# Kernel tuning notes

Measured on AMD Instinct MI355X. Metric: run time of the kernel, lower is better.

Reference implementation:

```python
import math
import jax, jax.numpy as jnp
import numpy as np

B, L, S, H, E, D = 4, 2048, 2048, 8, 64, 64

def setup_inputs() -> dict:
    key = jax.random.key(0)
    kq, kk, kv = jax.random.split(key, 3)
    return {
        "queries": jax.random.normal(kq, (B, L, H, E), dtype=jnp.float32),
        "keys": jax.random.normal(kk, (B, S, H, E), dtype=jnp.float32),
        "values": jax.random.normal(kv, (B, S, H, D), dtype=jnp.float32),
    }

def reference(queries, keys, values):
    E_ = queries.shape[-1]
    scale = 1.0 / math.sqrt(E_)
    # scores: [B, H, L, S]
    scores = jnp.einsum('blhe,bshe->bhls', queries, keys)
    A = jax.nn.softmax(scale * scores, axis=-1)
    # dropout omitted (eval mode / p=0.0)
    out = jnp.einsum('bhls,bshd->blhd', A, values)
    return out
```

## Files before the change

kernel.cpp:

```cpp
#include <hip/hip_runtime.h>
#include <hip/hip_bf16.h>


#define BNUM 4
#define LLEN 2048
#define SLEN 2048
#define HNUM 8
#define EDIM 64

typedef __attribute__((ext_vector_type(8))) short s16x8;
typedef __attribute__((ext_vector_type(8))) _Float16 hf16x8;
typedef __attribute__((ext_vector_type(2))) __fp16 fp16x2;
typedef __attribute__((ext_vector_type(4))) float f32x4;

__device__ __forceinline__ short f2h(float f) {
    union { _Float16 h; short s; } u;
    u.h = (_Float16)f;
    return u.s;
}

__device__ __forceinline__ s16x8 pk8(float4 a, float4 b) {
    union { fp16x2 h[4]; s16x8 v; } u;
    u.h[0] = __builtin_amdgcn_cvt_pkrtz(a.x, a.y);
    u.h[1] = __builtin_amdgcn_cvt_pkrtz(a.z, a.w);
    u.h[2] = __builtin_amdgcn_cvt_pkrtz(b.x, b.y);
    u.h[3] = __builtin_amdgcn_cvt_pkrtz(b.z, b.w);
    return u.v;
}

#if __has_builtin(__builtin_amdgcn_global_load_lds)
#define HAVE_GLL 1
#else
#define HAVE_GLL 0
#endif

__device__ __forceinline__ void stage16(const short* g, short* l) {
#if HAVE_GLL
    __builtin_amdgcn_global_load_lds(
        (const __attribute__((address_space(1))) void*)g,
        (__attribute__((address_space(3))) void*)l, 16, 0, 0);
#else
    *(s16x8*)l = *(const s16x8*)g;
#endif
}

__global__ __launch_bounds__(256)
void prep(const float* __restrict__ Kg, const float* __restrict__ Vg,
          short* __restrict__ Kc, short* __restrict__ Vt)
{
    __shared__ short tile[EDIM][80];
    if (blockIdx.y == 0) {
        const int t = blockIdx.x * 256 + threadIdx.x;
        const int e8 = t & 7;
        const int tmp = t >> 3;
        const int h = tmp & 7;
        const int tmp2 = tmp >> 3;
        const int s = tmp2 & (SLEN - 1);
        const int b = tmp2 >> 11;
        const float4* src = (const float4*)(Kg + (((size_t)(b * SLEN + s) * HNUM + h) * EDIM + e8 * 8));
        float4 a = src[0], bb = src[1];
        *(s16x8*)(Kc + ((size_t)((b * HNUM + h) * SLEN + s) * EDIM + e8 * 8)) = pk8(a, bb);
    } else {
        if (blockIdx.x >= 1024) return;
        const int x = blockIdx.x;
        const int s0 = (x & 31) * 64;
        const int bh = x >> 5;
        const int b = bh >> 3, h = bh & 7;
        {
            const int sr = threadIdx.x >> 2, dc = (threadIdx.x & 3) * 16;
            const float4* src = (const float4*)(Vg + (((size_t)(b * SLEN + s0 + sr) * HNUM + h) * EDIM + dc));
            #pragma unroll
            for (int j4 = 0; j4 < 4; ++j4) {
                float4 a = src[j4];
                tile[dc + j4*4 + 0][sr] = f2h(a.x);
                tile[dc + j4*4 + 1][sr] = f2h(a.y);
                tile[dc + j4*4 + 2][sr] = f2h(a.z);
                tile[dc + j4*4 + 3][sr] = f2h(a.w);
            }
        }
        __syncthreads();
        {
            const int dr = threadIdx.x >> 2, sc = (threadIdx.x & 3) * 16;
            short* dst = Vt + ((size_t)((b * HNUM + h) * EDIM + dr) * SLEN + s0 + sc);
            *(s16x8*)dst       = *(const s16x8*)&tile[dr][sc];
            *(s16x8*)(dst + 8) = *(const s16x8*)&tile[dr][sc + 8];
        }
    }
}

__global__ __launch_bounds__(512, 4)
void fa_fwd(const float* __restrict__ Qg, const short* __restrict__ Kc,
            const short* __restrict__ Vt, float* __restrict__ Og)
{
    __shared__ float sOf[128 * 68];
    __shared__ float sL[2][128];
    short* sKV = (short*)sOf;

    const int tid  = threadIdx.x;
    const int wave = tid >> 6;
    const int sw   = wave & 1;
    const int qh   = wave >> 1;
    const int lane = tid & 63;
    const int m    = lane & 15;
    const int quad = lane >> 4;

    const int lin  = (int)blockIdx.x;
    const int logi = ((lin & 7) << 6) + (lin >> 3);
    const int qx = logi & 15;
    const int h  = (logi >> 4) & 7;
    const int b  = logi >> 7;
    const int qbase = qx * 128;
    const int bh = b * HNUM + h;

    const short* Kbh = Kc + (size_t)bh * SLEN * EDIM;
    const short* Vbh = Vt + (size_t)bh * EDIM * SLEN;

    const int l3 = lane >> 3;
    const int ksrcE = (wave * 32 + l3) * EDIM + ((lane & 7) ^ (l3 & 3)) * 8;
    const int ksrcO = (wave * 32 + l3) * EDIM + ((lane & 7) ^ (4 + (l3 & 3))) * 8;
    const int vsrcB = (lane >> 2) * SLEN + wave * 32 + ((lane & 3) ^ ((lane >> 2) & 3)) * 8;
    short* kdstB = sKV + (wave * 256 + lane) * 8;
    short* vdstB = sKV + 4096 + (wave * 256 + lane) * 8;

#define STAGE_TILE(s0)                                                        \
    do {                                                                      \
        _Pragma("unroll")                                                     \
        for (int p = 0; p < 4; ++p) {                                         \
            const int ks = ((p & 1) ? ksrcO : ksrcE) + (p >> 1) * 1024 + (p & 1) * 512; \
            stage16(Kbh + (size_t)(s0) * EDIM + ks, kdstB + p * 512);         \
            stage16(Vbh + (s0) + vsrcB + p * 16 * SLEN, vdstB + p * 512);     \
        }                                                                     \
    } while (0)

    const float csc = 0.18033688011112042f;
    hf16x8 qfrag[2][2];
    #pragma unroll
    for (int qtl = 0; qtl < 2; ++qtl)
        #pragma unroll
        for (int kb = 0; kb < 2; ++kb) {
            const int qtg = qh * 2 + qtl;
            const float* qp = Qg + ((size_t)(b * LLEN + qbase + qtg * 16 + m) * HNUM + h) * EDIM
                              + kb * 32 + quad * 8;
            float4 x0 = *(const float4*)qp;
            float4 x1 = *(const float4*)(qp + 4);
            float4 y0 = {x0.x*csc, x0.y*csc, x0.z*csc, x0.w*csc};
            float4 y1 = {x1.x*csc, x1.y*csc, x1.z*csc, x1.w*csc};
            union { s16x8 s; hf16x8 hh; } u;
            u.s = pk8(y0, y1);
            qfrag[qtl][kb] = u.hh;
        }

    const int gk  = ((m >> 2) & 1) * 4 + (m & 3);
    const int pi0 = 8 * (m >> 2) + (m & 3);
    const int kOff00 = (sw * 32 + pi0)     * 64 + ((quad)     ^ gk) * 8;
    const int kOff01 = (sw * 32 + pi0)     * 64 + ((4 + quad) ^ gk) * 8;
    const int kOff10 = (sw * 32 + pi0 + 4) * 64 + ((quad)     ^ gk) * 8;
    const int kOff11 = (sw * 32 + pi0 + 4) * 64 + ((4 + quad) ^ gk) * 8;
    const int vOffB  = 4096 + sw * 2048 + m * 32 + ((quad ^ (m & 3)) * 8);

    hf16x8 vones;
    #pragma unroll
    for (int j = 0; j < 8; ++j) vones[j] = (_Float16)1.0f;

    f32x4 oacc[2][4];
    f32x4 lacc[2];
    #pragma unroll
    for (int i = 0; i < 2; ++i) {
        #pragma unroll
        for (int j = 0; j < 4; ++j) oacc[i][j] = (f32x4){0.f, 0.f, 0.f, 0.f};
        lacc[i] = (f32x4){0.f, 0.f, 0.f, 0.f};
    }

    if (wave < 2) STAGE_TILE(0);
    __syncthreads();

    for (int s0 = 0; s0 < SLEN; s0 += 64) {
        hf16x8 kf00 = *(const hf16x8*)(sKV + kOff00);
        hf16x8 kf01 = *(const hf16x8*)(sKV + kOff01);
        hf16x8 kf10 = *(const hf16x8*)(sKV + kOff10);
        hf16x8 kf11 = *(const hf16x8*)(sKV + kOff11);
        hf16x8 vf0 = *(const hf16x8*)(sKV + vOffB);
        hf16x8 vf1 = *(const hf16x8*)(sKV + vOffB + 512);
        hf16x8 vf2 = *(const hf16x8*)(sKV + vOffB + 1024);
        hf16x8 vf3 = *(const hf16x8*)(sKV + vOffB + 1536);

        __syncthreads();

        if (s0 + 64 < SLEN && wave < 2) STAGE_TILE(s0 + 64);

        #pragma unroll
        for (int qtl = 0; qtl < 2; ++qtl) {
            f32x4 a0 = {0.f, 0.f, 0.f, 0.f};
            f32x4 a1 = {0.f, 0.f, 0.f, 0.f};
            a0 = __builtin_amdgcn_mfma_f32_16x16x32_f16(kf00, qfrag[qtl][0], a0, 0, 0, 0);
            a0 = __builtin_amdgcn_mfma_f32_16x16x32_f16(kf01, qfrag[qtl][1], a0, 0, 0, 0);
            a1 = __builtin_amdgcn_mfma_f32_16x16x32_f16(kf10, qfrag[qtl][0], a1, 0, 0, 0);
            a1 = __builtin_amdgcn_mfma_f32_16x16x32_f16(kf11, qfrag[qtl][1], a1, 0, 0, 0);
            float p0 = __builtin_amdgcn_exp2f(a0[0]);
            float p1 = __builtin_amdgcn_exp2f(a0[1]);
            float p2 = __builtin_amdgcn_exp2f(a0[2]);
            float p3 = __builtin_amdgcn_exp2f(a0[3]);
            float p4 = __builtin_amdgcn_exp2f(a1[0]);
            float p5 = __builtin_amdgcn_exp2f(a1[1]);
            float p6 = __builtin_amdgcn_exp2f(a1[2]);
            float p7 = __builtin_amdgcn_exp2f(a1[3]);
            union { fp16x2 h2[4]; hf16x8 v; } pu;
            pu.h2[0] = __builtin_amdgcn_cvt_pkrtz(p0, p1);
            pu.h2[1] = __builtin_amdgcn_cvt_pkrtz(p2, p3);
            pu.h2[2] = __builtin_amdgcn_cvt_pkrtz(p4, p5);
            pu.h2[3] = __builtin_amdgcn_cvt_pkrtz(p6, p7);
            hf16x8 pf = pu.v;
            lacc[qtl] = __builtin_amdgcn_mfma_f32_16x16x32_f16(pf, vones, lacc[qtl], 0, 0, 0);
            oacc[qtl][0] = __builtin_amdgcn_mfma_f32_16x16x32_f16(pf, vf0, oacc[qtl][0], 0, 0, 0);
            oacc[qtl][1] = __builtin_amdgcn_mfma_f32_16x16x32_f16(pf, vf1, oacc[qtl][1], 0, 0, 0);
            oacc[qtl][2] = __builtin_amdgcn_mfma_f32_16x16x32_f16(pf, vf2, oacc[qtl][2], 0, 0, 0);
            oacc[qtl][3] = __builtin_amdgcn_mfma_f32_16x16x32_f16(pf, vf3, oacc[qtl][3], 0, 0, 0);
        }

        __syncthreads();
    }

    if (m == 0) {
        #pragma unroll
        for (int qtl = 0; qtl < 2; ++qtl)
            #pragma unroll
            for (int r = 0; r < 4; ++r)
                sL[sw][(qh * 2 + qtl) * 16 + quad * 4 + r] = lacc[qtl][r];
    }
    __syncthreads();

    if (sw == 0) {
        #pragma unroll
        for (int qtl = 0; qtl < 2; ++qtl)
            #pragma unroll
            for (int dt = 0; dt < 4; ++dt)
                #pragma unroll
                for (int r = 0; r < 4; ++r)
                    sOf[((qh * 2 + qtl) * 16 + quad * 4 + r) * 68 + dt * 16 + m] = oacc[qtl][dt][r];
    }
    __syncthreads();
    if (sw == 1) {
        #pragma unroll
        for (int qtl = 0; qtl < 2; ++qtl)
            #pragma unroll
            for (int dt = 0; dt < 4; ++dt)
                #pragma unroll
                for (int r = 0; r < 4; ++r)
                    sOf[((qh * 2 + qtl) * 16 + quad * 4 + r) * 68 + dt * 16 + m] += oacc[qtl][dt][r];
    }
    __syncthreads();

    {
        const int q = tid >> 2;
        const int dcol = (tid & 3) * 16;
        const float l = sL[0][q] + sL[1][q];
        const float inv = 1.0f / l;
        float* orow = Og + ((size_t)(b * LLEN + qbase + q) * HNUM + h) * EDIM + dcol;
        #pragma unroll
        for (int j = 0; j < 4; ++j) {
            float4 v = *(const float4*)(sOf + q * 68 + dcol + j * 4);
            v.x *= inv; v.y *= inv; v.z *= inv; v.w *= inv;
            *(float4*)(orow + j * 4) = v;
        }
    }
}

extern "C" void kernel_launch(void* const* d_in, const int* in_sizes, int n_in,
                              void* d_out, int out_size, void* d_ws, size_t ws_size,
                              hipStream_t stream) {
    const float* Q = (const float*)d_in[0];
    const float* K = (const float*)d_in[1];
    const float* V = (const float*)d_in[2];
    float* O = (float*)d_out;

    const size_t NE = (size_t)BNUM * LLEN * HNUM * EDIM;
    short* Kc = (short*)d_ws;
    short* Vt = Kc + NE;

    prep<<<dim3(2048, 2), dim3(256), 0, stream>>>(K, V, Kc, Vt);
    fa_fwd<<<dim3(512), dim3(512), 0, stream>>>(Q, Kc, Vt, O);
}
```

Before: 137.4 us.

## Fuse K/V fp16 conversion and V transpose into attention kernel, drop prep pass

```diff
diff --git a/kernel.cpp b/kernel.cpp
--- a/kernel.cpp
+++ b/kernel.cpp
@@ -7,6 +7,7 @@
 #define SLEN 2048
 #define HNUM 8
 #define EDIM 64
+#define RSTRIDE (HNUM * EDIM)
 
 typedef __attribute__((ext_vector_type(8))) short s16x8;
 typedef __attribute__((ext_vector_type(8))) _Float16 hf16x8;
@@ -28,69 +29,9 @@
     return u.v;
 }
 
-#if __has_builtin(__builtin_amdgcn_global_load_lds)
-#define HAVE_GLL 1
-#else
-#define HAVE_GLL 0
-#endif
-
-__device__ __forceinline__ void stage16(const short* g, short* l) {
-#if HAVE_GLL
-    __builtin_amdgcn_global_load_lds(
-        (const __attribute__((address_space(1))) void*)g,
-        (__attribute__((address_space(3))) void*)l, 16, 0, 0);
-#else
-    *(s16x8*)l = *(const s16x8*)g;
-#endif
-}
-
-__global__ __launch_bounds__(256)
-void prep(const float* __restrict__ Kg, const float* __restrict__ Vg,
-          short* __restrict__ Kc, short* __restrict__ Vt)
-{
-    __shared__ short tile[EDIM][80];
-    if (blockIdx.y == 0) {
-        const int t = blockIdx.x * 256 + threadIdx.x;
-        const int e8 = t & 7;
-        const int tmp = t >> 3;
-        const int h = tmp & 7;
-        const int tmp2 = tmp >> 3;
-        const int s = tmp2 & (SLEN - 1);
-        const int b = tmp2 >> 11;
-        const float4* src = (const float4*)(Kg + (((size_t)(b * SLEN + s) * HNUM + h) * EDIM + e8 * 8));
-        float4 a = src[0], bb = src[1];
-        *(s16x8*)(Kc + ((size_t)((b * HNUM + h) * SLEN + s) * EDIM + e8 * 8)) = pk8(a, bb);
-    } else {
-        if (blockIdx.x >= 1024) return;
-        const int x = blockIdx.x;
-        const int s0 = (x & 31) * 64;
-        const int bh = x >> 5;
-        const int b = bh >> 3, h = bh & 7;
-        {
-            const int sr = threadIdx.x >> 2, dc = (threadIdx.x & 3) * 16;
-            const float4* src = (const float4*)(Vg + (((size_t)(b * SLEN + s0 + sr) * HNUM + h) * EDIM + dc));
-            #pragma unroll
-            for (int j4 = 0; j4 < 4; ++j4) {
-                float4 a = src[j4];
-                tile[dc + j4*4 + 0][sr] = f2h(a.x);
-                tile[dc + j4*4 + 1][sr] = f2h(a.y);
-                tile[dc + j4*4 + 2][sr] = f2h(a.z);
-                tile[dc + j4*4 + 3][sr] = f2h(a.w);
-            }
-        }
-        __syncthreads();
-        {
-            const int dr = threadIdx.x >> 2, sc = (threadIdx.x & 3) * 16;
-            short* dst = Vt + ((size_t)((b * HNUM + h) * EDIM + dr) * SLEN + s0 + sc);
-            *(s16x8*)dst       = *(const s16x8*)&tile[dr][sc];
-            *(s16x8*)(dst + 8) = *(const s16x8*)&tile[dr][sc + 8];
-        }
-    }
-}
-
 __global__ __launch_bounds__(512, 4)
-void fa_fwd(const float* __restrict__ Qg, const short* __restrict__ Kc,
-            const short* __restrict__ Vt, float* __restrict__ Og)
+void fa_fwd(const float* __restrict__ Qg, const float* __restrict__ Kg,
+            const float* __restrict__ Vg, float* __restrict__ Og)
 {
     __shared__ float sOf[128 * 68];
     __shared__ float sL[2][128];
@@ -110,26 +51,41 @@
     const int h  = (logi >> 4) & 7;
     const int b  = logi >> 7;
     const int qbase = qx * 128;
-    const int bh = b * HNUM + h;
-
-    const short* Kbh = Kc + (size_t)bh * SLEN * EDIM;
-    const short* Vbh = Vt + (size_t)bh * EDIM * SLEN;
-
-    const int l3 = lane >> 3;
-    const int ksrcE = (wave * 32 + l3) * EDIM + ((lane & 7) ^ (l3 & 3)) * 8;
-    const int ksrcO = (wave * 32 + l3) * EDIM + ((lane & 7) ^ (4 + (l3 & 3))) * 8;
-    const int vsrcB = (lane >> 2) * SLEN + wave * 32 + ((lane & 3) ^ ((lane >> 2) & 3)) * 8;
-    short* kdstB = sKV + (wave * 256 + lane) * 8;
-    short* vdstB = sKV + 4096 + (wave * 256 + lane) * 8;
-
-#define STAGE_TILE(s0)                                                        \
+
+    const int srow = tid >> 3;
+    const int c8   = tid & 7;
+    const int gsw  = ((srow >> 3) & 1) * 4 + (srow & 3);
+    const int kdst = srow * 64 + ((c8 ^ gsw) * 8);
+    const int vbase0 = 4096 + ((srow >> 5) * 2048) + (srow & 7);
+    const int s3 = (srow >> 3) & 3;
+
+    const size_t rowOff = ((size_t)(b * SLEN + srow) * HNUM + h) * EDIM + c8 * 8;
+    const float* kRow = Kg + rowOff;
+    const float* vRow = Vg + rowOff;
+
+    float4 kg0, kg1, vg0, vg1;
+
+#define STAGE_LOAD(S0)                                                        \
     do {                                                                      \
-        _Pragma("unroll")                                                     \
-        for (int p = 0; p < 4; ++p) {                                         \
-            const int ks = ((p & 1) ? ksrcO : ksrcE) + (p >> 1) * 1024 + (p & 1) * 512; \
-            stage16(Kbh + (size_t)(s0) * EDIM + ks, kdstB + p * 512);         \
-            stage16(Vbh + (s0) + vsrcB + p * 16 * SLEN, vdstB + p * 512);     \
-        }                                                                     \
+        const float* kp = kRow + (size_t)(S0) * RSTRIDE;                      \
+        const float* vp = vRow + (size_t)(S0) * RSTRIDE;                      \
+        kg0 = ((const float4*)kp)[0];                                         \
+        kg1 = ((const float4*)kp)[1];                                         \
+        vg0 = ((const float4*)vp)[0];                                         \
+        vg1 = ((const float4*)vp)[1];                                         \
+    } while (0)
+
+#define STAGE_WRITE()                                                         \
+    do {                                                                      \
+        *(s16x8*)(sKV + kdst) = pk8(kg0, kg1);                                \
+        sKV[vbase0 + (c8 * 8 + 0) * 32 + ((s3 ^ 0) * 8)] = f2h(vg0.x);        \
+        sKV[vbase0 + (c8 * 8 + 1) * 32 + ((s3 ^ 1) * 8)] = f2h(vg0.y);        \
+        sKV[vbase0 + (c8 * 8 + 2) * 32 + ((s3 ^ 2) * 8)] = f2h(vg0.z);        \
+        sKV[vbase0 + (c8 * 8 + 3) * 32 + ((s3 ^ 3) * 8)] = f2h(vg0.w);        \
+        sKV[vbase0 + (c8 * 8 + 4) * 32 + ((s3 ^ 0) * 8)] = f2h(vg1.x);        \
+        sKV[vbase0 + (c8 * 8 + 5) * 32 + ((s3 ^ 1) * 8)] = f2h(vg1.y);        \
+        sKV[vbase0 + (c8 * 8 + 6) * 32 + ((s3 ^ 2) * 8)] = f2h(vg1.z);        \
+        sKV[vbase0 + (c8 * 8 + 7) * 32 + ((s3 ^ 3) * 8)] = f2h(vg1.w);        \
     } while (0)
 
     const float csc = 0.18033688011112042f;
@@ -171,7 +127,8 @@
         lacc[i] = (f32x4){0.f, 0.f, 0.f, 0.f};
     }
 
-    if (wave < 2) STAGE_TILE(0);
+    STAGE_LOAD(0);
+    STAGE_WRITE();
     __syncthreads();
 
     for (int s0 = 0; s0 < SLEN; s0 += 64) {
@@ -186,7 +143,8 @@
 
         __syncthreads();
 
-        if (s0 + 64 < SLEN && wave < 2) STAGE_TILE(s0 + 64);
+        const bool more = (s0 + 64 < SLEN);
+        if (more) STAGE_LOAD(s0 + 64);
 
         #pragma unroll
         for (int qtl = 0; qtl < 2; ++qtl) {
@@ -217,6 +175,8 @@
             oacc[qtl][3] = __builtin_amdgcn_mfma_f32_16x16x32_f16(pf, vf3, oacc[qtl][3], 0, 0, 0);
         }
 
+        if (more) STAGE_WRITE();
+
         __syncthreads();
     }
 
@@ -273,10 +233,5 @@
     const float* V = (const float*)d_in[2];
     float* O = (float*)d_out;
 
-    const size_t NE = (size_t)BNUM * LLEN * HNUM * EDIM;
-    short* Kc = (short*)d_ws;
-    short* Vt = Kc + NE;
-
-    prep<<<dim3(2048, 2), dim3(256), 0, stream>>>(K, V, Kc, Vt);
-    fa_fwd<<<dim3(512), dim3(512), 0, stream>>>(Q, Kc, Vt, O);
-}
+    fa_fwd<<<dim3(512), dim3(512), 0, stream>>>(Q, K, V, O);
+}
```

Result: slower. 142.0 us (+3.4%).

## Double-buffer K/V tiles in LDS and registers with one barrier per tile

Applied to the files above, without the earlier changes.

```diff
diff --git a/kernel.cpp b/kernel.cpp
--- a/kernel.cpp
+++ b/kernel.cpp
@@ -122,13 +122,15 @@
     short* kdstB = sKV + (wave * 256 + lane) * 8;
     short* vdstB = sKV + 4096 + (wave * 256 + lane) * 8;
 
-#define STAGE_TILE(s0)                                                        \
+#define STAGE_TILE(BUFO, s0)                                                  \
     do {                                                                      \
+        short* kd = kdstB + (BUFO);                                           \
+        short* vd = vdstB + (BUFO);                                           \
         _Pragma("unroll")                                                     \
         for (int p = 0; p < 4; ++p) {                                         \
             const int ks = ((p & 1) ? ksrcO : ksrcE) + (p >> 1) * 1024 + (p & 1) * 512; \
-            stage16(Kbh + (size_t)(s0) * EDIM + ks, kdstB + p * 512);         \
-            stage16(Vbh + (s0) + vsrcB + p * 16 * SLEN, vdstB + p * 512);     \
+            stage16(Kbh + (size_t)(s0) * EDIM + ks, kd + p * 512);            \
+            stage16(Vbh + (s0) + vsrcB + p * 16 * SLEN, vd + p * 512);        \
         }                                                                     \
     } while (0)
 
@@ -158,6 +160,18 @@
     const int kOff11 = (sw * 32 + pi0 + 4) * 64 + ((4 + quad) ^ gk) * 8;
     const int vOffB  = 4096 + sw * 2048 + m * 32 + ((quad ^ (m & 3)) * 8);
 
+#define READ_FRAGS(K00, K01, K10, K11, V0, V1, V2, V3, BUFO)                  \
+    do {                                                                      \
+        K00 = *(const hf16x8*)(sKV + (BUFO) + kOff00);                        \
+        K01 = *(const hf16x8*)(sKV + (BUFO) + kOff01);                        \
+        K10 = *(const hf16x8*)(sKV + (BUFO) + kOff10);                        \
+        K11 = *(const hf16x8*)(sKV + (BUFO) + kOff11);                        \
+        V0  = *(const hf16x8*)(sKV + (BUFO) + vOffB);                         \
+        V1  = *(const hf16x8*)(sKV + (BUFO) + vOffB + 512);                   \
+        V2  = *(const hf16x8*)(sKV + (BUFO) + vOffB + 1024);                  \
+        V3  = *(const hf16x8*)(sKV + (BUFO) + vOffB + 1536);                  \
+    } while (0)
+
     hf16x8 vones;
     #pragma unroll
     for (int j = 0; j < 8; ++j) vones[j] = (_Float16)1.0f;
@@ -171,53 +185,67 @@
         lacc[i] = (f32x4){0.f, 0.f, 0.f, 0.f};
     }
 
-    if (wave < 2) STAGE_TILE(0);
+#define COMPUTE(K00, K01, K10, K11, V0, V1, V2, V3)                           \
+    do {                                                                      \
+        _Pragma("unroll")                                                     \
+        for (int qtl = 0; qtl < 2; ++qtl) {                                   \
+            f32x4 a0 = {0.f, 0.f, 0.f, 0.f};                                  \
+            f32x4 a1 = {0.f, 0.f, 0.f, 0.f};                                  \
+            a0 = __builtin_amdgcn_mfma_f32_16x16x32_f16(K00, qfrag[qtl][0], a0, 0, 0, 0); \
+            a0 = __builtin_amdgcn_mfma_f32_16x16x32_f16(K01, qfrag[qtl][1], a0, 0, 0, 0); \
+            a1 = __builtin_amdgcn_mfma_f32_16x16x32_f16(K10, qfrag[qtl][0], a1, 0, 0, 0); \
+            a1 = __builtin_amdgcn_mfma_f32_16x16x32_f16(K11, qfrag[qtl][1], a1, 0, 0, 0); \
+            float p0 = __builtin_amdgcn_exp2f(a0[0]);                         \
+            float p1 = __builtin_amdgcn_exp2f(a0[1]);                         \
+            float p2 = __builtin_amdgcn_exp2f(a0[2]);                         \
+            float p3 = __builtin_amdgcn_exp2f(a0[3]);                         \
+            float p4 = __builtin_amdgcn_exp2f(a1[0]);                         \
+            float p5 = __builtin_amdgcn_exp2f(a1[1]);                         \
+            float p6 = __builtin_amdgcn_exp2f(a1[2]);                         \
+            float p7 = __builtin_amdgcn_exp2f(a1[3]);                         \
+            union { fp16x2 h2[4]; hf16x8 v; } pu;                             \
+            pu.h2[0] = __builtin_amdgcn_cvt_pkrtz(p0, p1);                    \
+            pu.h2[1] = __builtin_amdgcn_cvt_pkrtz(p2, p3);                    \
+            pu.h2[2] = __builtin_amdgcn_cvt_pkrtz(p4, p5);                    \
+            pu.h2[3] = __builtin_amdgcn_cvt_pkrtz(p6, p7);                    \
+            hf16x8 pf = pu.v;                                                 \
+            lacc[qtl] = __builtin_amdgcn_mfma_f32_16x16x32_f16(pf, vones, lacc[qtl], 0, 0, 0); \
+            oacc[qtl][0] = __builtin_amdgcn_mfma_f32_16x16x32_f16(pf, V0, oacc[qtl][0], 0, 0, 0); \
+            oacc[qtl][1] = __builtin_amdgcn_mfma_f32_16x16x32_f16(pf, V1, oacc[qtl][1], 0, 0, 0); \
+            oacc[qtl][2] = __builtin_amdgcn_mfma_f32_16x16x32_f16(pf, V2, oacc[qtl][2], 0, 0, 0); \
+            oacc[qtl][3] = __builtin_amdgcn_mfma_f32_16x16x32_f16(pf, V3, oacc[qtl][3], 0, 0, 0); \
+        }                                                                     \
+    } while (0)
+
+    hf16x8 kA00, kA01, kA10, kA11, vA0, vA1, vA2, vA3;
+    hf16x8 kB00, kB01, kB10, kB11, vB0, vB1, vB2, vB3;
+
+    if (wave < 2) STAGE_TILE(0, 0);
+    asm volatile("s_waitcnt vmcnt(0)" ::: "memory");
     __syncthreads();
-
-    for (int s0 = 0; s0 < SLEN; s0 += 64) {
-        hf16x8 kf00 = *(const hf16x8*)(sKV + kOff00);
-        hf16x8 kf01 = *(const hf16x8*)(sKV + kOff01);
-        hf16x8 kf10 = *(const hf16x8*)(sKV + kOff10);
-        hf16x8 kf11 = *(const hf16x8*)(sKV + kOff11);
-        hf16x8 vf0 = *(const hf16x8*)(sKV + vOffB);
-        hf16x8 vf1 = *(const hf16x8*)(sKV + vOffB + 512);
-        hf16x8 vf2 = *(const hf16x8*)(sKV + vOffB + 1024);
-        hf16x8 vf3 = *(const hf16x8*)(sKV + vOffB + 1536);
-
-        __syncthreads();
-
-        if (s0 + 64 < SLEN && wave < 2) STAGE_TILE(s0 + 64);
-
-        #pragma unroll
-        for (int qtl = 0; qtl < 2; ++qtl) {
-            f32x4 a0 = {0.f, 0.f, 0.f, 0.f};
-            f32x4 a1 = {0.f, 0.f, 0.f, 0.f};
-            a0 = __builtin_amdgcn_mfma_f32_16x16x32_f16(kf00, qfrag[qtl][0], a0, 0, 0, 0);
-            a0 = __builtin_amdgcn_mfma_f32_16x16x32_f16(kf01, qfrag[qtl][1], a0, 0, 0, 0);
-            a1 = __builtin_amdgcn_mfma_f32_16x16x32_f16(kf10, qfrag[qtl][0], a1, 0, 0, 0);
-            a1 = __builtin_amdgcn_mfma_f32_16x16x32_f16(kf11, qfrag[qtl][1], a1, 0, 0, 0);
-            float p0 = __builtin_amdgcn_exp2f(a0[0]);
-            float p1 = __builtin_amdgcn_exp2f(a0[1]);
-            float p2 = __builtin_amdgcn_exp2f(a0[2]);
-            float p3 = __builtin_amdgcn_exp2f(a0[3]);
-            float p4 = __builtin_amdgcn_exp2f(a1[0]);
-            float p5 = __builtin_amdgcn_exp2f(a1[1]);
-            float p6 = __builtin_amdgcn_exp2f(a1[2]);
-            float p7 = __builtin_amdgcn_exp2f(a1[3]);
-            union { fp16x2 h2[4]; hf16x8 v; } pu;
-            pu.h2[0] = __builtin_amdgcn_cvt_pkrtz(p0, p1);
-            pu.h2[1] = __builtin_amdgcn_cvt_pkrtz(p2, p3);
-            pu.h2[2] = __builtin_amdgcn_cvt_pkrtz(p4, p5);
-            pu.h2[3] = __builtin_amdgcn_cvt_pkrtz(p6, p7);
-            hf16x8 pf = pu.v;
-            lacc[qtl] = __builtin_amdgcn_mfma_f32_16x16x32_f16(pf, vones, lacc[qtl], 0, 0, 0);
-            oacc[qtl][0] = __builtin_amdgcn_mfma_f32_16x16x32_f16(pf, vf0, oacc[qtl][0], 0, 0, 0);
-            oacc[qtl][1] = __builtin_amdgcn_mfma_f32_16x16x32_f16(pf, vf1, oacc[qtl][1], 0, 0, 0);
-            oacc[qtl][2] = __builtin_amdgcn_mfma_f32_16x16x32_f16(pf, vf2, oacc[qtl][2], 0, 0, 0);
-            oacc[qtl][3] = __builtin_amdgcn_mfma_f32_16x16x32_f16(pf, vf3, oacc[qtl][3], 0, 0, 0);
-        }
-
-        __syncthreads();
+    READ_FRAGS(kA00, kA01, kA10, kA11, vA0, vA1, vA2, vA3, 0);
+    if (wave < 2) STAGE_TILE(8192, 64);
+
+    for (int t = 0; t < 32; t += 2) {
+        asm volatile("s_waitcnt lgkmcnt(0) vmcnt(0)" ::: "memory");
+        __builtin_amdgcn_sched_barrier(0);
+        __builtin_amdgcn_s_barrier();
+        READ_FRAGS(kB00, kB01, kB10, kB11, vB0, vB1, vB2, vB3, 8192);
+        if (t + 2 < 32 && wave < 2) STAGE_TILE(0, (t + 2) * 64);
+        __builtin_amdgcn_s_setprio(1);
+        COMPUTE(kA00, kA01, kA10, kA11, vA0, vA1, vA2, vA3);
+        __builtin_amdgcn_s_setprio(0);
+
+        asm volatile("s_waitcnt lgkmcnt(0) vmcnt(0)" ::: "memory");
+        __builtin_amdgcn_sched_barrier(0);
+        __builtin_amdgcn_s_barrier();
+        if (t + 2 < 32) {
+            READ_FRAGS(kA00, kA01, kA10, kA11, vA0, vA1, vA2, vA3, 0);
+            if (t + 3 < 32 && wave < 2) STAGE_TILE(8192, (t + 3) * 64);
+        }
+        __builtin_amdgcn_s_setprio(1);
+        COMPUTE(kB00, kB01, kB10, kB11, vB0, vB1, vB2, vB3);
+        __builtin_amdgcn_s_setprio(0);
     }
 
     if (m == 0) {
```

After: 338.0 us. +146.0%, slower.
